# Performance work log

Hardware: AMD Instinct MI355X
Metric: run time of the kernel (lower is better)

The kernel has to match this reference:

```python
import jax, jax.numpy as jnp
import numpy as np

EMBED_DIM = 1024
NUM_HEADS = 16
HEAD_DIM = EMBED_DIM // NUM_HEADS
BITS = 8


def quantize_bits(x, bits):
    # Faithful min-max fake quantization from the original module.
    qmax = 2 ** bits - 1
    x_min = x.min()
    x_max = x.max()
    scale = (x_max - x_min) / (qmax + 1e-08)
    x_q = jnp.round(jnp.clip((x - x_min) / (scale + 1e-08), 0, qmax))
    return x_q * scale + x_min


def rope_sin_cos(seq_len, dim):
    # inv_freq over half the head dim, matching RotaryEmbedding's freqs table.
    inv_freq = 1.0 / 10000 ** (jnp.arange(0, dim, 2, dtype=jnp.float32) / dim)
    t = jnp.arange(seq_len, dtype=jnp.float32)
    freqs = t[:, None] * inv_freq[None, :]  # (S, D/2)
    return jnp.sin(freqs), jnp.cos(freqs)


def apply_rotary(x, sin, cos):
    # x: (B, H, S, D); sin/cos: (1, 1, S, D/2)
    x1, x2 = jnp.split(x, 2, axis=-1)
    return jnp.concatenate([x1 * cos - x2 * sin, x1 * sin + x2 * cos], axis=-1)


def setup_inputs() -> dict:
    key = jax.random.key(0)
    k1, k2, k3 = jax.random.split(key, 3)
    B, S, E = 2, 2048, EMBED_DIM
    x = jax.random.normal(k1, (B, S, E), dtype=jnp.float32)
    # lecun_normal-style init: std = 1/sqrt(fan_in)
    w_qkv = jax.random.normal(k2, (E, 3 * E), dtype=jnp.float32) / np.sqrt(E)
    w_out = jax.random.normal(k3, (E, E), dtype=jnp.float32) / np.sqrt(E)
    return {"x": x, "w_qkv": w_qkv, "w_out": w_out}


def reference(x, w_qkv, w_out):
    B, S, E = x.shape
    H, D = NUM_HEADS, HEAD_DIM
    # Fake-quantized QKV projection
    qkv = x @ quantize_bits(w_qkv, BITS)                    # (B, S, 3E)
    qkv = qkv.reshape(B, S, 3, H, D)
    q = qkv[:, :, 0].transpose(0, 2, 1, 3)                  # (B, H, S, D)
    k = qkv[:, :, 1].transpose(0, 2, 1, 3)
    v = qkv[:, :, 2].transpose(0, 2, 1, 3)
    sin, cos = rope_sin_cos(S, D)
    sin = sin[None, None]
    cos = cos[None, None]
    q = apply_rotary(q, sin, cos)
    k = apply_rotary(k, sin, cos)
    scores = jnp.einsum('bhqd,bhkd->bhqk', q, k) / jnp.sqrt(jnp.float32(D))
    attn = jax.nn.softmax(scores, axis=-1)                  # (B, H, S, S)
    out = jnp.einsum('bhqk,bhkd->bhqd', attn, v)            # (B, H, S, D)
    out = out.transpose(0, 2, 1, 3).reshape(B, S, E)
    return out @ quantize_bits(w_out, BITS)
```

## Files before the change

kernel.cpp:

```cpp
#include <hip/hip_runtime.h>
#include <hip/hip_bf16.h>

typedef __bf16 bf16;
typedef bf16  bf16x8 __attribute__((ext_vector_type(8)));
typedef bf16  bf16x4 __attribute__((ext_vector_type(4)));
typedef bf16  bf16x2 __attribute__((ext_vector_type(2)));
typedef float f32x4  __attribute__((ext_vector_type(4)));
typedef float f32x16 __attribute__((ext_vector_type(16)));
typedef int   i32x4  __attribute__((ext_vector_type(4)));

#define MFMA16(a,b,c) __builtin_amdgcn_mfma_f32_16x16x32_bf16((a),(b),(c),0,0,0)
#define MFMA32(a,b,c) __builtin_amdgcn_mfma_f32_32x32x16_bf16((a),(b),(c),0,0,0)

#define GLDS16(gp, lp) __builtin_amdgcn_global_load_lds( \
    (const __attribute__((address_space(1))) void*)(void*)(gp), \
    (__attribute__((address_space(3))) void*)(lp), 16, 0, 0)

static __device__ __forceinline__ bf16x8 lds_frag(const char* p){
  i32x4 v = *(const i32x4*)p;
  return __builtin_bit_cast(bf16x8, v);
}
static __device__ __forceinline__ bf16x8 g_frag(const bf16* p){
  i32x4 v = *(const i32x4*)p;
  return __builtin_bit_cast(bf16x8, v);
}
static __device__ __forceinline__ unsigned pk_bf16(float a, float b){
  bf16x2 v = { (bf16)a, (bf16)b };
  return __builtin_bit_cast(unsigned, v);
}
static __device__ __forceinline__ void p32swap(unsigned &a, unsigned &b){
  asm("v_permlane32_swap_b32 %0, %1" : "+v"(a), "+v"(b));
}
static __device__ __forceinline__ float max3(float a, float b, float c){
  return fmaxf(fmaxf(a, b), c);
}

__device__ __forceinline__ unsigned fmap(float f){
  unsigned u = __float_as_uint(f);
  return (u & 0x80000000u) ? ~u : (u | 0x80000000u);
}
__device__ __forceinline__ float funmap(unsigned m){
  unsigned u = (m & 0x80000000u) ? (m & 0x7FFFFFFFu) : ~m;
  return __uint_as_float(u);
}

__global__ void init_mm(unsigned* mm){
  if (threadIdx.x == 0){
    mm[0] = 0xFFFFFFFFu; mm[1] = 0u;
    mm[2] = 0xFFFFFFFFu; mm[3] = 0u;
  }
}

__global__ void minmax_k(const float* __restrict__ w, int n, unsigned* __restrict__ mm){
  __shared__ unsigned smn[256], smx[256];
  int tid = threadIdx.x;
  unsigned lmn = 0xFFFFFFFFu, lmx = 0u;
  for (int i = blockIdx.x * blockDim.x + tid; i < n; i += gridDim.x * blockDim.x){
    unsigned u = fmap(w[i]);
    lmn = min(lmn, u); lmx = max(lmx, u);
  }
  smn[tid] = lmn; smx[tid] = lmx;
  __syncthreads();
  for (int s = 128; s > 0; s >>= 1){
    if (tid < s){
      smn[tid] = min(smn[tid], smn[tid + s]);
      smx[tid] = max(smx[tid], smx[tid + s]);
    }
    __syncthreads();
  }
  if (tid == 0){ atomicMin(&mm[0], smn[0]); atomicMax(&mm[1], smx[0]); }
}

__global__ void dq_t(const float* __restrict__ w, bf16* __restrict__ wt,
                     int R, int C, const unsigned* __restrict__ mm){
  __shared__ float t[32][33];
  float xmin = funmap(mm[0]);
  float xmax = funmap(mm[1]);
  float scale = (xmax - xmin) / 255.0f;
  float denom = scale + 1e-8f;
  int ct = blockIdx.x * 32, rt = blockIdx.y * 32;
  int tx = threadIdx.x, ty = threadIdx.y;
#pragma unroll
  for (int p = 0; p < 4; ++p){
    int r = rt + p * 8 + ty;
    float x = w[(size_t)r * C + ct + tx];
    float q = rintf(fminf(fmaxf((x - xmin) / denom, 0.0f), 255.0f));
    t[p * 8 + ty][tx] = q * scale + xmin;
  }
  __syncthreads();
#pragma unroll
  for (int p = 0; p < 4; ++p){
    int c = p * 8 + ty;
    wt[(size_t)(ct + c) * R + rt + tx] = (bf16)t[tx][c];
  }
}

__global__ void cast_x(const float* __restrict__ x, bf16* __restrict__ xb, int n4){
  int i = blockIdx.x * 256 + threadIdx.x;
  if (i < n4){
    f32x4 v = *(const f32x4*)(x + (size_t)i * 4);
    bf16x4 o = { (bf16)v.x, (bf16)v.y, (bf16)v.z, (bf16)v.w };
    *(bf16x4*)(xb + (size_t)i * 4) = o;
  }
}

__global__ void sincos_k(float2* __restrict__ sctab){
  int idx = blockIdx.x * 256 + threadIdx.x;
  int i = idx & 31, s = idx >> 5;
  float invf = powf(10000.0f, -(float)i / 32.0f);
  float fr = (float)s * invf;
  float2 cs; cs.x = cosf(fr); cs.y = sinf(fr);
  sctab[idx] = cs;
}

__global__ __launch_bounds__(256, 2) void gemm_bt(
    const bf16* __restrict__ A, const bf16* __restrict__ Bt,
    float* __restrict__ C, int M, int N, int K)
{
  __shared__ __align__(16) char lds[32768];
  int nbx = N >> 7;
  int bid = blockIdx.x;
  int nwg = gridDim.x;
  if ((nwg & 7) == 0){ int q = nwg >> 3; bid = (bid & 7) * q + (bid >> 3); }
  int row0 = (bid / nbx) << 7;
  int col0 = (bid % nbx) << 7;
  int tid = threadIdx.x, lane = tid & 63, wid = tid >> 6;
  int wr = (wid >> 1) * 64, wc = (wid & 1) * 64;
  int lr = lane & 15, g = lane >> 4;

  int aoff[2][4], boff[2][4];
#pragma unroll
  for (int kk = 0; kk < 2; ++kk){
#pragma unroll
    for (int m = 0; m < 4; ++m){
      int ra = wr + m * 16 + lr;
      aoff[kk][m] = ra * 128 + ((((kk * 4 + g) ^ ((ra >> 1) & 7))) << 4);
      int rb = wc + m * 16 + lr;
      boff[kk][m] = 16384 + rb * 128 + ((((kk * 4 + g) ^ ((rb >> 1) & 7))) << 4);
    }
  }

  const bf16* pA[4]; const bf16* pB[4]; int loff[4];
#pragma unroll
  for (int is = 0; is < 4; ++is){
    int f = is * 4096 + wid * 1024 + lane * 16;
    int r = f >> 7, c = (f >> 4) & 7;
    int cg = c ^ ((r >> 1) & 7);
    pA[is] = A  + (size_t)(row0 + r) * K + cg * 8;
    pB[is] = Bt + (size_t)(col0 + r) * K + cg * 8;
    loff[is] = is * 4096 + wid * 1024;
  }

  f32x4 acc[4][4] = {};
  for (int kt = 0; kt < K; kt += 64){
    __syncthreads();
#pragma unroll
    for (int is = 0; is < 4; ++is){
      GLDS16(pA[is] + kt, lds + loff[is]);
      GLDS16(pB[is] + kt, lds + 16384 + loff[is]);
    }
    __syncthreads();
#pragma unroll
    for (int kk = 0; kk < 2; ++kk){
      bf16x8 af[4], bfb[4];
#pragma unroll
      for (int m = 0; m < 4; ++m) af[m] = lds_frag(lds + aoff[kk][m]);
#pragma unroll
      for (int n = 0; n < 4; ++n) bfb[n] = lds_frag(lds + boff[kk][n]);
#pragma unroll
      for (int m = 0; m < 4; ++m)
#pragma unroll
        for (int n = 0; n < 4; ++n)
          acc[m][n] = MFMA16(af[m], bfb[n], acc[m][n]);
    }
  }

#pragma unroll
  for (int m = 0; m < 4; ++m){
    int row = row0 + wr + m * 16 + g * 4;
#pragma unroll
    for (int n = 0; n < 4; ++n){
      int col = col0 + wc + n * 16 + lr;
      float* cp = C + (size_t)row * N + col;
#pragma unroll
      for (int r = 0; r < 4; ++r)
        cp[(size_t)r * N] = acc[m][n][r];
    }
  }
}

__global__ __launch_bounds__(256, 2) void gemm_qkv(
    const bf16* __restrict__ A, const bf16* __restrict__ Bt,
    const float2* __restrict__ sctab,
    bf16* __restrict__ Qr, bf16* __restrict__ Kr, bf16* __restrict__ Vt,
    int M, int N, int K)
{
  __shared__ __align__(16) char lds[32768];
  int nbx = N >> 7;
  int bid = blockIdx.x;
  int nwg = gridDim.x;
  if ((nwg & 7) == 0){ int q = nwg >> 3; bid = (bid & 7) * q + (bid >> 3); }
  int row0 = (bid / nbx) << 7;
  int col0 = (bid % nbx) << 7;
  int tid = threadIdx.x, lane = tid & 63, wid = tid >> 6;
  int wr = (wid >> 1) * 64, wc = (wid & 1) * 64;
  int lr = lane & 15, g = lane >> 4;

  int aoff[2][4], boff[2][4];
#pragma unroll
  for (int kk = 0; kk < 2; ++kk){
#pragma unroll
    for (int m = 0; m < 4; ++m){
      int ra = wr + m * 16 + lr;
      aoff[kk][m] = ra * 128 + ((((kk * 4 + g) ^ ((ra >> 1) & 7))) << 4);
      int rb = wc + m * 16 + lr;
      boff[kk][m] = 16384 + rb * 128 + ((((kk * 4 + g) ^ ((rb >> 1) & 7))) << 4);
    }
  }

  const bf16* pA[4]; const bf16* pB[4]; int loff[4];
#pragma unroll
  for (int is = 0; is < 4; ++is){
    int f = is * 4096 + wid * 1024 + lane * 16;
    int r = f >> 7, c = (f >> 4) & 7;
    int cg = c ^ ((r >> 1) & 7);
    pA[is] = A  + (size_t)(row0 + r) * K + cg * 8;
    pB[is] = Bt + (size_t)(col0 + r) * K + cg * 8;
    loff[is] = is * 4096 + wid * 1024;
  }

  f32x4 acc[4][4] = {};
  for (int kt = 0; kt < K; kt += 64){
    __syncthreads();
#pragma unroll
    for (int is = 0; is < 4; ++is){
      GLDS16(pA[is] + kt, lds + loff[is]);
      GLDS16(pB[is] + kt, lds + 16384 + loff[is]);
    }
    __syncthreads();
#pragma unroll
    for (int kk = 0; kk < 2; ++kk){
      bf16x8 af[4], bfb[4];
#pragma unroll
      for (int m = 0; m < 4; ++m) af[m] = lds_frag(lds + aoff[kk][m]);
#pragma unroll
      for (int n = 0; n < 4; ++n) bfb[n] = lds_frag(lds + boff[kk][n]);
#pragma unroll
      for (int m = 0; m < 4; ++m)
#pragma unroll
        for (int n = 0; n < 4; ++n)
          acc[m][n] = MFMA16(af[m], bfb[n], acc[m][n]);
    }
  }

  int head = (col0 + wc) >> 6;
  int sect = head >> 4;
  int h = head & 15;
  const float QS = 0.18033688011f;

  if (sect == 2){
#pragma unroll
    for (int m = 0; m < 4; ++m){
      int s = row0 + wr + m * 16 + g * 4;
      int b = s >> 11, s2 = s & 2047;
#pragma unroll
      for (int n = 0; n < 4; ++n){
        int d = n * 16 + lr;
        bf16x4 v4 = { (bf16)acc[m][n][0], (bf16)acc[m][n][1],
                      (bf16)acc[m][n][2], (bf16)acc[m][n][3] };
        *(bf16x4*)(Vt + (((size_t)(b * 16 + h)) * 64 + d) * 2048 + s2) = v4;
      }
    }
  } else {
    bf16* dst = sect ? Kr : Qr;
    float scl = sect ? 1.0f : QS;
#pragma unroll
    for (int m = 0; m < 4; ++m){
#pragma unroll
      for (int r = 0; r < 4; ++r){
        int s = row0 + wr + m * 16 + g * 4 + r;
        int b = s >> 11, s2 = s & 2047;
        bf16* qp = dst + (((size_t)(b * 16 + h)) * 2048 + s2) * 64;
#pragma unroll
        for (int n = 0; n < 2; ++n){
          float x1 = acc[m][n][r], x2 = acc[m][n + 2][r];
          float2 cs = sctab[s2 * 32 + n * 16 + lr];
          qp[n * 16 + lr]      = (bf16)((x1 * cs.x - x2 * cs.y) * scl);
          qp[n * 16 + lr + 32] = (bf16)((x1 * cs.y + x2 * cs.x) * scl);
        }
      }
    }
  }
}

__global__ __launch_bounds__(256, 4) void attn_k(
    const bf16* __restrict__ Q, const bf16* __restrict__ K,
    const bf16* __restrict__ Vt, bf16* __restrict__ AO)
{
  __shared__ __align__(16) char SB[32768];

  int bid = blockIdx.x;
  bid = (bid & 7) * 128 + (bid >> 3);
  int bh = bid >> 5, qb = bid & 31;
  int b = bh >> 4, h = bh & 15;
  int tid = threadIdx.x, lane = tid & 63, wid = tid >> 6;
  int l31 = lane & 31, hi = lane >> 5, hi8 = hi * 8;
  int qt = wid >> 1, half = wid & 1;
  int q0 = qb * 64 + qt * 32;

  const bf16* Qb = Q  + ((size_t)bh * 2048 + q0) * 64;
  const bf16* Kb = K  + (size_t)bh * 2048 * 64;
  const bf16* Vb = Vt + (size_t)bh * 64 * 2048;
  const bf16* Kh = Kb + (size_t)half * 1024 * 64;
  int vcol0 = half * 1024;

  bf16x8 qf[4];
#pragma unroll
  for (int t = 0; t < 4; ++t)
    qf[t] = g_frag(Qb + (size_t)l31 * 64 + t * 16 + hi8);

  const bf16* pKs[4]; const bf16* pVs[4]; int ldo[4];
#pragma unroll
  for (int is = 0; is < 4; ++is){
    int f = qt * 4096 + is * 1024 + lane * 16;
    int r = f >> 7;
    int cg = ((f >> 4) & 7) ^ (r & 7);
    pKs[is] = Kh + (size_t)r * 64 + cg * 8;
    pVs[is] = Vb + (size_t)r * 2048 + vcol0 + cg * 8;
    ldo[is] = qt * 4096 + is * 1024;
  }
  char* klh = SB + half * 8192;
  char* vlh = SB + 16384 + half * 8192;

  f32x16 o0 = {}, o1 = {};
  float mrun = -1e30f, lrun = 0.0f;

  for (int c = 0; c < 16; ++c){
    int kv0 = c * 64;
    __syncthreads();
#pragma unroll
    for (int is = 0; is < 4; ++is){
      GLDS16(pKs[is] + (size_t)kv0 * 64, klh + ldo[is]);
      GLDS16(pVs[is] + kv0,              vlh + ldo[is]);
    }
    __syncthreads();

#pragma unroll
    for (int kk = 0; kk < 2; ++kk){
      int krow = kk * 32 + l31;
      bf16x8 kf[4], vfr[4];
#pragma unroll
      for (int t = 0; t < 4; ++t)
        kf[t] = lds_frag(klh + krow * 128 + ((((2 * t + hi) ^ (krow & 7))) << 4));
#pragma unroll
      for (int u = 0; u < 4; ++u){
        int d = (u & 1) * 32 + l31;
        vfr[u] = lds_frag(vlh + d * 128 +
                          ((((kk * 4) + ((u >> 1) * 2) + hi) ^ (d & 7)) << 4));
      }
      f32x16 sc = {};
#pragma unroll
      for (int t = 0; t < 4; ++t) sc = MFMA32(kf[t], qf[t], sc);

      float t0 = max3(sc[0], sc[1], sc[2]);
      float t1 = max3(sc[3], sc[4], sc[5]);
      float t2 = max3(sc[6], sc[7], sc[8]);
      float t3 = max3(sc[9], sc[10], sc[11]);
      float t4 = max3(sc[12], sc[13], sc[14]);
      float mt = fmaxf(max3(t0, t1, t2), max3(t3, t4, sc[15]));
      if (!__all(mt - mrun <= 8.0f)){
        mt = fmaxf(mt, __shfl_xor(mt, 32));
        float mn = fmaxf(mrun, mt);
        float cr = __builtin_amdgcn_exp2f(mrun - mn);
#pragma unroll
        for (int r = 0; r < 16; ++r){ o0[r] *= cr; o1[r] *= cr; }
        lrun *= cr; mrun = mn;
      }
#pragma unroll
      for (int r = 0; r < 16; ++r) sc[r] = __builtin_amdgcn_exp2f(sc[r] - mrun);
      float s0 = (sc[0] + sc[1]) + (sc[2] + sc[3]);
      float s1 = (sc[4] + sc[5]) + (sc[6] + sc[7]);
      float s2 = (sc[8] + sc[9]) + (sc[10] + sc[11]);
      float s3 = (sc[12] + sc[13]) + (sc[14] + sc[15]);
      lrun += (s0 + s1) + (s2 + s3);

#pragma unroll
      for (int kh = 0; kh < 2; ++kh){
        unsigned pa0 = pk_bf16(sc[kh * 8 + 0], sc[kh * 8 + 1]);
        unsigned pa1 = pk_bf16(sc[kh * 8 + 2], sc[kh * 8 + 3]);
        unsigned pb0 = pk_bf16(sc[kh * 8 + 4], sc[kh * 8 + 5]);
        unsigned pb1 = pk_bf16(sc[kh * 8 + 6], sc[kh * 8 + 7]);
        p32swap(pa0, pb0); p32swap(pa1, pb1);
        i32x4 wv = { (int)pa0, (int)pa1, (int)pb0, (int)pb1 };
        bf16x8 pf = __builtin_bit_cast(bf16x8, wv);
        o0 = MFMA32(vfr[kh * 2 + 0], pf, o0);
        o1 = MFMA32(vfr[kh * 2 + 1], pf, o1);
      }
    }
  }

  lrun += __shfl_xor(lrun, 32);

  __syncthreads();
  float* ml = (float*)SB;
  if (lane < 32){ ml[wid * 64 + l31] = mrun; ml[wid * 64 + 32 + l31] = lrun; }
  __syncthreads();
  float mp = ml[(wid ^ 1) * 64 + l31];
  float lp = ml[(wid ^ 1) * 64 + 32 + l31];
  __syncthreads();
  float M = fmaxf(mrun, mp);
  float ew = __builtin_amdgcn_exp2f(mrun - M);
  float ep = __builtin_amdgcn_exp2f(mp - M);
  float inv = ew / (lrun * ew + lp * ep);
  float* Ow = (float*)SB + wid * 2048;
#pragma unroll
  for (int r = 0; r < 16; ++r){
    int d = 8 * (r >> 2) + 4 * hi + (r & 3);
    Ow[d * 32 + l31]        = o0[r] * inv;
    Ow[(d + 32) * 32 + l31] = o1[r] * inv;
  }
  __syncthreads();
  int qt2 = tid >> 7, qf31 = tid & 31, dseg = (tid >> 5) & 3;
  const float* Oa = (float*)SB + (2 * qt2) * 2048;
  const float* Ob = (float*)SB + (2 * qt2 + 1) * 2048;
  bf16* outp = AO + ((size_t)(b * 2048 + qb * 64 + qt2 * 32 + qf31)) * 1024
                  + h * 64 + dseg * 16;
  bf16x8 w0, w1;
#pragma unroll
  for (int j = 0; j < 8; ++j){
    int d = dseg * 16 + j;
    w0[j] = (bf16)(Oa[d * 32 + qf31] + Ob[d * 32 + qf31]);
  }
#pragma unroll
  for (int j = 0; j < 8; ++j){
    int d = dseg * 16 + 8 + j;
    w1[j] = (bf16)(Oa[d * 32 + qf31] + Ob[d * 32 + qf31]);
  }
  *(bf16x8*)outp = w0;
  *(bf16x8*)(outp + 8) = w1;
}

extern "C" void kernel_launch(void* const* d_in, const int* in_sizes, int n_in,
                              void* d_out, int out_size, void* d_ws, size_t ws_size,
                              hipStream_t stream) {
  const float* x     = (const float*)d_in[0];
  const float* w_qkv = (const float*)d_in[1];
  const float* w_out = (const float*)d_in[2];
  float* out = (float*)d_out;

  char* ws = (char*)d_ws;
  const size_t MB = 1u << 20;
  unsigned* mm   = (unsigned*)(ws);
  float2* sctab  = (float2*)(ws + 256);
  bf16* xb       = (bf16*)(ws + 1 * MB);
  bf16* wqkvT    = (bf16*)(ws + 9 * MB);
  bf16* woutT    = (bf16*)(ws + 15 * MB);
  bf16* Qr       = (bf16*)(ws + 65 * MB);
  bf16* Kr       = (bf16*)(ws + 73 * MB);
  bf16* Vt       = (bf16*)(ws + 81 * MB);
  bf16* AO       = (bf16*)(ws + 1 * MB);

  init_mm<<<1, 64, 0, stream>>>(mm);
  minmax_k<<<512, 256, 0, stream>>>(w_qkv, 1024 * 3072, mm);
  minmax_k<<<512, 256, 0, stream>>>(w_out, 1024 * 1024, mm + 2);
  sincos_k<<<256, 256, 0, stream>>>(sctab);
  cast_x<<<4096, 256, 0, stream>>>(x, xb, 4194304 / 4);
  dq_t<<<dim3(96, 32), dim3(32, 8), 0, stream>>>(w_qkv, wqkvT, 1024, 3072, mm);
  dq_t<<<dim3(32, 32), dim3(32, 8), 0, stream>>>(w_out, woutT, 1024, 1024, mm + 2);
  gemm_qkv<<<768, 256, 0, stream>>>(xb, wqkvT, sctab, Qr, Kr, Vt, 4096, 3072, 1024);
  attn_k<<<1024, 256, 0, stream>>>(Qr, Kr, Vt, AO);
  gemm_bt<<<256, 256, 0, stream>>>(AO, woutT, out, 4096, 1024, 1024);

  (void)in_sizes; (void)n_in; (void)out_size; (void)ws_size;
}
```

Measured before the change: 157.4 us.

## Double-buffer K/V tiles in attention loop with smaller 32-key chunks

The attention kernel now loads K and V in 32-key chunks into two LDS buffers per half and prefetches the next chunk while computing on the current one. This replaces the previous scheme of 64-key chunks with two barriers per iteration. The V tile layout in LDS changes to match, and LDS fragment offsets are precomputed outside the loop. The aim is to hide global-to-LDS load latency behind MFMA and softmax work and to halve the barriers per chunk. The cost is more iterations, each carrying a barrier, and reliance on async LDS loads finishing before the next barrier.

```diff
diff --git a/kernel.cpp b/kernel.cpp
--- a/kernel.cpp
+++ b/kernel.cpp
@@ -309,9 +309,8 @@
   int q0 = qb * 64 + qt * 32;
 
   const bf16* Qb = Q  + ((size_t)bh * 2048 + q0) * 64;
-  const bf16* Kb = K  + (size_t)bh * 2048 * 64;
+  const bf16* Kh = K  + (size_t)bh * 2048 * 64 + (size_t)half * 1024 * 64;
   const bf16* Vb = Vt + (size_t)bh * 64 * 2048;
-  const bf16* Kh = Kb + (size_t)half * 1024 * 64;
   int vcol0 = half * 1024;
 
   bf16x8 qf[4];
@@ -319,89 +318,99 @@
   for (int t = 0; t < 4; ++t)
     qf[t] = g_frag(Qb + (size_t)l31 * 64 + t * 16 + hi8);
 
-  const bf16* pKs[4]; const bf16* pVs[4]; int ldo[4];
-#pragma unroll
-  for (int is = 0; is < 4; ++is){
-    int f = qt * 4096 + is * 1024 + lane * 16;
+  const bf16* pKs[2]; const bf16* pVs[2]; int ldo[2];
+#pragma unroll
+  for (int is = 0; is < 2; ++is){
+    int f = qt * 2048 + is * 1024 + lane * 16;
     int r = f >> 7;
     int cg = ((f >> 4) & 7) ^ (r & 7);
     pKs[is] = Kh + (size_t)r * 64 + cg * 8;
-    pVs[is] = Vb + (size_t)r * 2048 + vcol0 + cg * 8;
-    ldo[is] = qt * 4096 + is * 1024;
-  }
-  char* klh = SB + half * 8192;
-  char* vlh = SB + 16384 + half * 8192;
+    int d = (cg < 4) ? r : r + 32;
+    int ko = (cg & 3) * 8;
+    pVs[is] = Vb + (size_t)d * 2048 + vcol0 + ko;
+    ldo[is] = qt * 2048 + is * 1024;
+  }
+  char* base = SB + half * 16384;
 
   f32x16 o0 = {}, o1 = {};
   float mrun = -1e30f, lrun = 0.0f;
 
-  for (int c = 0; c < 16; ++c){
-    int kv0 = c * 64;
-    __syncthreads();
-#pragma unroll
-    for (int is = 0; is < 4; ++is){
-      GLDS16(pKs[is] + (size_t)kv0 * 64, klh + ldo[is]);
-      GLDS16(pVs[is] + kv0,              vlh + ldo[is]);
-    }
-    __syncthreads();
-
-#pragma unroll
-    for (int kk = 0; kk < 2; ++kk){
-      int krow = kk * 32 + l31;
-      bf16x8 kf[4], vfr[4];
-#pragma unroll
-      for (int t = 0; t < 4; ++t)
-        kf[t] = lds_frag(klh + krow * 128 + ((((2 * t + hi) ^ (krow & 7))) << 4));
-#pragma unroll
-      for (int u = 0; u < 4; ++u){
-        int d = (u & 1) * 32 + l31;
-        vfr[u] = lds_frag(vlh + d * 128 +
-                          ((((kk * 4) + ((u >> 1) * 2) + hi) ^ (d & 7)) << 4));
+  int koff[4], voff[4];
+#pragma unroll
+  for (int t = 0; t < 4; ++t)
+    koff[t] = l31 * 128 + (((2 * t + hi) ^ (l31 & 7)) << 4);
+#pragma unroll
+  for (int u = 0; u < 4; ++u)
+    voff[u] = 4096 + l31 * 128 + ((((u & 1) * 4 + (u >> 1) * 2 + hi) ^ (l31 & 7)) << 4);
+
+#pragma unroll
+  for (int is = 0; is < 2; ++is){
+    GLDS16(pKs[is], base + ldo[is]);
+    GLDS16(pVs[is], base + 4096 + ldo[is]);
+  }
+  __syncthreads();
+
+  for (int c = 0; c < 32; ++c){
+    int cur = (c & 1) << 13;
+    if (c < 31){
+      int nxt = ((c + 1) & 1) << 13;
+      int kv0 = (c + 1) * 32;
+#pragma unroll
+      for (int is = 0; is < 2; ++is){
+        GLDS16(pKs[is] + (size_t)kv0 * 64, base + nxt + ldo[is]);
+        GLDS16(pVs[is] + kv0,              base + nxt + 4096 + ldo[is]);
       }
-      f32x16 sc = {};
-#pragma unroll
-      for (int t = 0; t < 4; ++t) sc = MFMA32(kf[t], qf[t], sc);
-
-      float t0 = max3(sc[0], sc[1], sc[2]);
-      float t1 = max3(sc[3], sc[4], sc[5]);
-      float t2 = max3(sc[6], sc[7], sc[8]);
-      float t3 = max3(sc[9], sc[10], sc[11]);
-      float t4 = max3(sc[12], sc[13], sc[14]);
-      float mt = fmaxf(max3(t0, t1, t2), max3(t3, t4, sc[15]));
-      if (!__all(mt - mrun <= 8.0f)){
-        mt = fmaxf(mt, __shfl_xor(mt, 32));
-        float mn = fmaxf(mrun, mt);
-        float cr = __builtin_amdgcn_exp2f(mrun - mn);
-#pragma unroll
-        for (int r = 0; r < 16; ++r){ o0[r] *= cr; o1[r] *= cr; }
-        lrun *= cr; mrun = mn;
-      }
-#pragma unroll
-      for (int r = 0; r < 16; ++r) sc[r] = __builtin_amdgcn_exp2f(sc[r] - mrun);
-      float s0 = (sc[0] + sc[1]) + (sc[2] + sc[3]);
-      float s1 = (sc[4] + sc[5]) + (sc[6] + sc[7]);
-      float s2 = (sc[8] + sc[9]) + (sc[10] + sc[11]);
-      float s3 = (sc[12] + sc[13]) + (sc[14] + sc[15]);
-      lrun += (s0 + s1) + (s2 + s3);
-
-#pragma unroll
-      for (int kh = 0; kh < 2; ++kh){
-        unsigned pa0 = pk_bf16(sc[kh * 8 + 0], sc[kh * 8 + 1]);
-        unsigned pa1 = pk_bf16(sc[kh * 8 + 2], sc[kh * 8 + 3]);
-        unsigned pb0 = pk_bf16(sc[kh * 8 + 4], sc[kh * 8 + 5]);
-        unsigned pb1 = pk_bf16(sc[kh * 8 + 6], sc[kh * 8 + 7]);
-        p32swap(pa0, pb0); p32swap(pa1, pb1);
-        i32x4 wv = { (int)pa0, (int)pa1, (int)pb0, (int)pb1 };
-        bf16x8 pf = __builtin_bit_cast(bf16x8, wv);
-        o0 = MFMA32(vfr[kh * 2 + 0], pf, o0);
-        o1 = MFMA32(vfr[kh * 2 + 1], pf, o1);
-      }
-    }
+    }
+    const char* bufp = base + cur;
+    bf16x8 kf[4], vfr[4];
+#pragma unroll
+    for (int t = 0; t < 4; ++t) kf[t] = lds_frag(bufp + koff[t]);
+#pragma unroll
+    for (int u = 0; u < 4; ++u) vfr[u] = lds_frag(bufp + voff[u]);
+
+    f32x16 sc = {};
+#pragma unroll
+    for (int t = 0; t < 4; ++t) sc = MFMA32(kf[t], qf[t], sc);
+
+    float t0 = max3(sc[0], sc[1], sc[2]);
+    float t1 = max3(sc[3], sc[4], sc[5]);
+    float t2 = max3(sc[6], sc[7], sc[8]);
+    float t3 = max3(sc[9], sc[10], sc[11]);
+    float t4 = max3(sc[12], sc[13], sc[14]);
+    float mt = fmaxf(max3(t0, t1, t2), max3(t3, t4, sc[15]));
+    if (!__all(mt - mrun <= 8.0f)){
+      mt = fmaxf(mt, __shfl_xor(mt, 32));
+      float mn = fmaxf(mrun, mt);
+      float cr = __builtin_amdgcn_exp2f(mrun - mn);
+#pragma unroll
+      for (int r = 0; r < 16; ++r){ o0[r] *= cr; o1[r] *= cr; }
+      lrun *= cr; mrun = mn;
+    }
+#pragma unroll
+    for (int r = 0; r < 16; ++r) sc[r] = __builtin_amdgcn_exp2f(sc[r] - mrun);
+    float s0 = (sc[0] + sc[1]) + (sc[2] + sc[3]);
+    float s1 = (sc[4] + sc[5]) + (sc[6] + sc[7]);
+    float s2 = (sc[8] + sc[9]) + (sc[10] + sc[11]);
+    float s3 = (sc[12] + sc[13]) + (sc[14] + sc[15]);
+    lrun += (s0 + s1) + (s2 + s3);
+
+#pragma unroll
+    for (int kh = 0; kh < 2; ++kh){
+      unsigned pa0 = pk_bf16(sc[kh * 8 + 0], sc[kh * 8 + 1]);
+      unsigned pa1 = pk_bf16(sc[kh * 8 + 2], sc[kh * 8 + 3]);
+      unsigned pb0 = pk_bf16(sc[kh * 8 + 4], sc[kh * 8 + 5]);
+      unsigned pb1 = pk_bf16(sc[kh * 8 + 6], sc[kh * 8 + 7]);
+      p32swap(pa0, pb0); p32swap(pa1, pb1);
+      i32x4 wv = { (int)pa0, (int)pa1, (int)pb0, (int)pb1 };
+      bf16x8 pf = __builtin_bit_cast(bf16x8, wv);
+      o0 = MFMA32(vfr[kh * 2 + 0], pf, o0);
+      o1 = MFMA32(vfr[kh * 2 + 1], pf, o1);
+    }
+    __syncthreads();
   }
 
   lrun += __shfl_xor(lrun, 32);
 
-  __syncthreads();
   float* ml = (float*)SB;
   if (lane < 32){ ml[wid * 64 + l31] = mrun; ml[wid * 64 + 32 + l31] = lrun; }
   __syncthreads();
```

New measurement: 158.1 us. About the same (+0.4%).
